# Performance work log

Measured on AMD Instinct MI355X. Metric: run time of the kernel, lower is better.

Reference implementation:

```python
import jax, jax.numpy as jnp
import numpy as np

H = W = 256
C = 128
SCALE = 512 ** (-0.5)  # literal from the source, not 1/sqrt(C)


def _pool_mat(size, out):
    # adaptive_avg_pool1d matrix: row i averages input[start_i:end_i]
    i = np.arange(out)
    s = (i * size) // out
    e = ((i + 1) * size + out - 1) // out  # ceil
    P = np.zeros((out, size), np.float32)
    for k in range(out):
        P[k, s[k]:e[k]] = 1.0 / (e[k] - s[k])
    return jnp.asarray(P)


def adaptive_avg_pool2d(x, out):
    # x: [B, C, H, W] -> [B, C, out, out] via separable pooling matrices
    Ph = _pool_mat(x.shape[2], out)
    Pw = _pool_mat(x.shape[3], out)
    y = jnp.einsum('oh,bchw->bcow', Ph, x)
    return jnp.einsum('pw,bcow->bcop', Pw, y)


def setup_inputs() -> dict:
    key = jax.random.key(0)
    k1, k2 = jax.random.split(key)
    x5 = jax.random.normal(k1, (4, C, H, W), dtype=jnp.float32)
    W_out = jax.random.normal(k2, (C, C), dtype=jnp.float32) * 0.02
    b_out = jnp.zeros((C,), dtype=jnp.float32)
    return {"x5": x5, "W_out": W_out, "b_out": b_out}


def reference(x5, W_out, b_out):
    B = x5.shape[0]
    # Query: [B, N, C], N = H*W
    Query = x5.reshape(B, C, H * W).transpose(0, 2, 1)
    # multi-scale pooled keys
    p16 = adaptive_avg_pool2d(x5, 16)
    p12 = adaptive_avg_pool2d(x5, 12)
    p9 = adaptive_avg_pool2d(x5, 9)
    p7 = adaptive_avg_pool2d(x5, 7)
    p6 = adaptive_avg_pool2d(x5, 6)
    p3 = adaptive_avg_pool2d(x5, 3)
    p1 = adaptive_avg_pool2d(x5, 1)
    # Key: concat flattened pools in source order [3, 1, 9, 7, 16] -> [B, C, 396]
    Key = jnp.concatenate(
        [p.reshape(B, C, -1) for p in (p3, p1, p9, p7, p16)], axis=-1)
    Value = Key.transpose(0, 2, 1)  # [B, 396, C]
    # attention: [B, N, 396]
    attn = jax.nn.softmax(SCALE * jnp.einsum('bnc,bck->bnk', Query, Key), axis=-1)
    agg = jnp.einsum('bnk,bkc->bnc', attn, Value)  # [B, N, C]
    agg = agg.transpose(0, 2, 1).reshape(B, C, H, W)
    # 1x1 conv
    out = jnp.einsum('oc,bchw->bohw', W_out, agg) + b_out[None, :, None, None]
    return (out + x5, p12, p6)
```

## Files before the change

### kernel.cpp

```cpp
#include <hip/hip_runtime.h>
#include <hip/hip_bf16.h>

typedef short bf16x8 __attribute__((ext_vector_type(8)));
typedef float f32x4  __attribute__((ext_vector_type(4)));
typedef unsigned short u16;

#define B_N 4
#define C_N 128
#define HW_ 256
#define NPIX 65536
#define NK 396
#define NKP 400
#define OUT_MAIN ((size_t)B_N * C_N * NPIX)
#define P12_OFF OUT_MAIN
#define P6_OFF  (P12_OFF + (size_t)B_N * C_N * 144)

#define BUFSZ  32768
#define VT_OFF 16384
#define LDS_BYTES 65536

static __device__ __forceinline__ u16 f2bf(float x) {
  __hip_bfloat16 h = __float2bfloat16(x);
  return *(u16*)&h;
}
static __device__ __forceinline__ unsigned pack2(float lo, float hi) {
  return ((unsigned)f2bf(hi) << 16) | f2bf(lo);
}
static __device__ __forceinline__ void gl_lds16(const void* g, void* l) {
  __builtin_amdgcn_global_load_lds(
      (const __attribute__((address_space(1))) unsigned*)g,
      (__attribute__((address_space(3))) unsigned*)l, 16, 0, 0);
}
#define MFMA32 __builtin_amdgcn_mfma_f32_16x16x32_bf16
#define BAR() do { __builtin_amdgcn_s_barrier(); \
                   __builtin_amdgcn_sched_barrier(0); } while (0)
#define VM8() do { asm volatile("s_waitcnt vmcnt(8)" ::: "memory"); \
                   __builtin_amdgcn_sched_barrier(0); } while (0)
#define VM4() do { asm volatile("s_waitcnt vmcnt(4)" ::: "memory"); \
                   __builtin_amdgcn_sched_barrier(0); } while (0)

template<int H0>
static __device__ __forceinline__ void pool_phaseA(
    const float2* __restrict__ plane2, float (*yh)[257], int w2)
{
  const int os_[7] = {16,12,9,7,6,3,1};
  const int ro_[7] = {0,16,28,37,44,50,53};
  float ax[7], ay[7], a2x[7], a2y[7], inv_[7];
  int r_[7], e_[7], s2_[7];
  #pragma unroll
  for (int s = 0; s < 7; ++s) {
    const int o = os_[s];
    const int r = (H0 * o) >> 8;
    const int sr = (r * 256) / o;
    r_[s]  = r;
    e_[s]  = ((r + 1) * 256 + o - 1) / o;
    s2_[s] = ((r + 1) * 256) / o;
    inv_[s] = 1.0f / (float)(e_[s] - sr);
    ax[s] = 0.f; ay[s] = 0.f; a2x[s] = 0.f; a2y[s] = 0.f;
  }
  #pragma unroll
  for (int g = 0; g < 4; ++g) {
    float2 vv[8];
    #pragma unroll
    for (int k = 0; k < 8; ++k) vv[k] = plane2[(H0 + g*8 + k) * 128 + w2];
    #pragma unroll
    for (int k = 0; k < 8; ++k) {
      const int h = H0 + g*8 + k;
      const float2 v = vv[k];
      #pragma unroll
      for (int s = 0; s < 7; ++s) {
        const int o = os_[s];
        ax[s] += v.x; ay[s] += v.y;
        if (h >= s2_[s]) { a2x[s] += v.x; a2y[s] += v.y; }
        if (h + 1 == e_[s]) {
          atomicAdd(&yh[ro_[s] + r_[s]][2*w2],     ax[s] * inv_[s]);
          atomicAdd(&yh[ro_[s] + r_[s]][2*w2 + 1], ay[s] * inv_[s]);
          r_[s]++;
          const int sr = s2_[s];
          e_[s]  = ((r_[s] + 1) * 256 + o - 1) / o;
          s2_[s] = ((r_[s] + 1) * 256) / o;
          inv_[s] = 1.0f / (float)(e_[s] - sr);
          ax[s] = a2x[s]; ay[s] = a2y[s];
          a2x[s] = 0.f; a2y[s] = 0.f;
        }
      }
    }
  }
  #pragma unroll
  for (int s = 0; s < 7; ++s) {
    const int o = os_[s];
    if (r_[s] < o) {
      atomicAdd(&yh[ro_[s] + r_[s]][2*w2],     ax[s] * inv_[s]);
      atomicAdd(&yh[ro_[s] + r_[s]][2*w2 + 1], ay[s] * inv_[s]);
      if (r_[s] + 1 < o && s2_[s] < H0 + 32) {
        const int sr2 = s2_[s];
        const int e2  = ((r_[s] + 2) * 256 + o - 1) / o;
        const float inv2 = 1.0f / (float)(e2 - sr2);
        atomicAdd(&yh[ro_[s] + r_[s] + 1][2*w2],     a2x[s] * inv2);
        atomicAdd(&yh[ro_[s] + r_[s] + 1][2*w2 + 1], a2y[s] * inv2);
      }
    }
  }
}

__global__ __launch_bounds__(1024) void pool_kernel(
    const float* __restrict__ x5, const float* __restrict__ W_out,
    u16* __restrict__ wsK, u16* __restrict__ wsKT, u16* __restrict__ wsW,
    float* __restrict__ out)
{
  __shared__ float yh[54][257];
  const int tid = threadIdx.x;
  const int bc = blockIdx.x;
  const int b  = bc >> 7;
  const int c  = bc & 127;
  const float2* plane2 = (const float2*)(x5 + (size_t)bc * NPIX);
  const int w2 = tid & 127;
  const int q  = tid >> 7;

  if (bc < 16) {
    const int idx = bc * 1024 + tid;
    const int o = idx >> 7, pp = idx & 127;
    const int q32 = pp >> 5, pos = pp & 31, g = pos >> 3, jj = pos & 7;
    const int csrc = q32 * 32 + ((jj < 4) ? (g * 4 + jj) : (16 + g * 4 + (jj - 4)));
    wsW[idx] = f2bf(W_out[o * 128 + csrc]);
  }

  for (int i = tid; i < 54 * 257; i += 1024) ((float*)yh)[i] = 0.f;
  __syncthreads();

  switch (q) {
    case 0: pool_phaseA<0>  (plane2, yh, w2); break;
    case 1: pool_phaseA<32> (plane2, yh, w2); break;
    case 2: pool_phaseA<64> (plane2, yh, w2); break;
    case 3: pool_phaseA<96> (plane2, yh, w2); break;
    case 4: pool_phaseA<128>(plane2, yh, w2); break;
    case 5: pool_phaseA<160>(plane2, yh, w2); break;
    case 6: pool_phaseA<192>(plane2, yh, w2); break;
    default: pool_phaseA<224>(plane2, yh, w2); break;
  }
  __syncthreads();

  if (tid < NKP - NK) {
    wsK [((size_t)b * NKP + NK + tid) * C_N + c] = 0;
    wsKT[(size_t)bc * NKP + NK + tid] = 0;
  }

  const int grp = tid >> 4;
  const int gl  = tid & 15;
  #pragma unroll
  for (int it = 0; it < 9; ++it) {
    const int r = grp + it * 64;
    int rr = r;
    int o, ro, kbase, dst;
    if      (rr < 256) { o = 16; ro = 0;  kbase = 140; dst = 0; }
    else if (rr < 400) { o = 12; ro = 16; kbase = 0;   dst = 1; rr -= 256; }
    else if (rr < 481) { o = 9;  ro = 28; kbase = 10;  dst = 0; rr -= 400; }
    else if (rr < 530) { o = 7;  ro = 37; kbase = 91;  dst = 0; rr -= 481; }
    else if (rr < 566) { o = 6;  ro = 44; kbase = 0;   dst = 2; rr -= 530; }
    else if (rr < 575) { o = 3;  ro = 50; kbase = 0;   dst = 0; rr -= 566; }
    else               { o = 1;  ro = 53; kbase = 9;   dst = 0; rr = 0;   }
    const int i = rr / o;
    const int j = rr - i * o;
    const int s = (j * HW_) / o;
    const int e = ((j + 1) * HW_ + o - 1) / o;
    float partial = 0.f;
    const float* row = yh[ro + i];
    for (int wq = s + gl; wq < e; wq += 16) partial += row[wq];
    partial += __shfl_xor(partial, 1);
    partial += __shfl_xor(partial, 2);
    partial += __shfl_xor(partial, 4);
    partial += __shfl_xor(partial, 8);
    if (gl == 0) {
      const float v = partial * (1.0f / (float)(e - s));
      if (dst == 1) {
        out[P12_OFF + (size_t)bc * 144 + rr] = v;
      } else if (dst == 2) {
        out[P6_OFF + (size_t)bc * 36 + rr] = v;
      } else {
        const int key = kbase + rr;
        const u16 bv = f2bf(v);
        wsK [((size_t)b * NKP + key) * C_N + c] = bv;
        wsKT[(size_t)bc * NKP + key]            = bv;
      }
    }
  }
}

template<int CB, int BUF>
static __device__ __forceinline__ void stage64(
    char* smem, const char* wsKb, const char* wsKTb, int wv, int lane)
{
  char* buf = smem + BUF * BUFSZ;
  const int lr = lane >> 4, lc = lane & 15;
  const int rit = wv * 4 + lr;
  #pragma unroll
  for (int j = 0; j < 4; ++j) {
    const int gk = CB + (j >> 1) * 32 + wv * 8 + ((j & 1) << 2) + lr;
    gl_lds16(wsKb + (size_t)gk * 256 + ((lc ^ rit) << 4),
             buf + j*4096 + wv*1024);
    const int vrow = j*32 + wv*8 + (lane >> 3);
    gl_lds16(wsKTb + (size_t)vrow * (NKP*2) + CB*2 + (((lane & 7) ^ (vrow & 7)) << 4),
             buf + VT_OFF + j*4096 + wv*1024);
  }
}

static __device__ __forceinline__ void stage_tail(
    char* buf, const char* wsKb, const char* wsKTb, int wv, int lane)
{
  const int lr = lane >> 4;
  const int rit = wv * 4 + lr;
  #pragma unroll
  for (int j = 0; j < 2; ++j) {
    const int gk = 384 + wv * 8 + (j << 2) + lr;
    gl_lds16(wsKb + (size_t)gk * 256 + (((lane & 15) ^ rit) << 4),
             buf + j*4096 + wv*1024);
  }
  #pragma unroll
  for (int j = 0; j < 2; ++j) {
    const int row = j*64 + wv*16 + (lane >> 2);
    gl_lds16(wsKTb + (size_t)row * (NKP*2) + 768 + ((lane & 3) << 4),
             buf + VT_OFF + j*4096 + wv*1024);
  }
}

static __device__ __forceinline__ void stage_W(
    char* smem, const u16* wsW, int wv, int lane)
{
  #pragma unroll
  for (int j = 0; j < 8; ++j) {
    const int row = j*16 + wv*4 + (lane >> 4);
    gl_lds16((const char*)wsW + (size_t)row * 256 + (((lane & 15) ^ (row & 15)) << 4),
             smem + BUFSZ + j*4096 + wv*1024);
  }
}

template<int BUF, int TAIL>
static __device__ __forceinline__ void compute64(
    char* smem, const bf16x8 (&qf)[2][4],
    f32x4 (&agg)[8][2], float (&d)[2], int l15, int l4)
{
  const char* buf = smem + BUF * BUFSZ;
  constexpr int NT   = TAIL ? 2 : 4;
  constexpr int SUBS = TAIL ? 1 : 2;

  f32x4 sA[NT][2];
  #pragma unroll
  for (int nt = 0; nt < NT; ++nt) {
    sA[nt][0] = (f32x4){0.f,0.f,0.f,0.f};
    sA[nt][1] = (f32x4){0.f,0.f,0.f,0.f};
  }
  #pragma unroll
  for (int nt = 0; nt < NT; ++nt) {
    bf16x8 kf[4];
    #pragma unroll
    for (int kc = 0; kc < 4; ++kc)
      kf[kc] = *(const bf16x8*)(buf + (nt*16 + l15) * 256 +
                                ((kc*64 + l4*16) ^ (l15 << 4)));
    #pragma unroll
    for (int kc = 0; kc < 4; ++kc) {
      sA[nt][0] = MFMA32(kf[kc], qf[0][kc], sA[nt][0], 0, 0, 0);
      sA[nt][1] = MFMA32(kf[kc], qf[1][kc], sA[nt][1], 0, 0, 0);
    }
  }

  #pragma unroll
  for (int sub = 0; sub < SUBS; ++sub) {
    bf16x8 pf[2];
    #pragma unroll
    for (int pt = 0; pt < 2; ++pt) {
      float e[8];
      #pragma unroll
      for (int qi = 0; qi < 4; ++qi) e[qi]     = exp2f(sA[2*sub][pt][qi]);
      #pragma unroll
      for (int qi = 0; qi < 4; ++qi) e[4 + qi] = exp2f(sA[2*sub + 1][pt][qi]);
      if (TAIL) {
        #pragma unroll
        for (int j = 0; j < 8; ++j) if (l4*8 + j >= 12) e[j] = 0.f;
      }
      d[pt] += ((e[0]+e[1]) + (e[2]+e[3])) + ((e[4]+e[5]) + (e[6]+e[7]));
      bf16x8 t;
      #pragma unroll
      for (int j = 0; j < 8; ++j) t[j] = (short)f2bf(e[j]);
      pf[pt] = t;
    }
    #pragma unroll
    for (int ct = 0; ct < 8; ++ct) {
      const int vrow = ct*16 + l15;
      bf16x8 vf;
      if (TAIL)
        vf = *(const bf16x8*)(buf + VT_OFF + vrow*64 + l4*16);
      else
        vf = *(const bf16x8*)(buf + VT_OFF + vrow*128 +
                              ((sub*64 + l4*16) ^ ((vrow & 7) << 4)));
      agg[ct][0] = MFMA32(vf, pf[0], agg[ct][0], 0, 0, 0);
      agg[ct][1] = MFMA32(vf, pf[1], agg[ct][1], 0, 0, 0);
    }
  }
}

__global__ __launch_bounds__(256, 2) void attn_kernel(
    const float* __restrict__ x5, const u16* __restrict__ wsK,
    const u16* __restrict__ wsKT, const u16* __restrict__ wsW,
    const float* __restrict__ b_out, float* __restrict__ out)
{
  extern __shared__ char smem[];
  const int tid  = threadIdx.x;
  const int wgid = (blockIdx.x & 7) * 256 + (blockIdx.x >> 3);
  const int b    = wgid >> 9;
  const int pix0 = (wgid & 511) << 7;
  const int lane = tid & 63, wv = tid >> 6;
  const int l15  = lane & 15, l4 = lane >> 4;
  const float SCL2 = 0.044194173824159216f * 1.4426950408889634f;

  const char* wsKb  = (const char*)wsK  + (size_t)b * NKP * C_N * 2;
  const char* wsKTb = (const char*)wsKT + (size_t)b * C_N * NKP * 2;

  {
    const float* r0p = x5 + (((size_t)(b * C_N + 2*lane)) << 16) + pix0 + wv * 32;
    const float* r1p = r0p + NPIX;
    float4 v0[8], v1[8];
    #pragma unroll
    for (int j = 0; j < 8; ++j) {
      v0[j] = *(const float4*)(r0p + j*4);
      v1[j] = *(const float4*)(r1p + j*4);
    }
    #pragma unroll
    for (int i = 0; i < 32; ++i) {
      const int pix = wv * 32 + i;
      const unsigned pk = pack2(((const float*)&v0[i>>2])[i&3] * SCL2,
                                ((const float*)&v1[i>>2])[i&3] * SCL2);
      *(unsigned*)(smem + pix * 256 + ((lane*4) ^ ((pix & 15) << 4))) = pk;
    }
  }
  __syncthreads();

  bf16x8 qf[2][4];
  #pragma unroll
  for (int pt = 0; pt < 2; ++pt)
    #pragma unroll
    for (int kc = 0; kc < 4; ++kc)
      qf[pt][kc] = *(const bf16x8*)(smem + (wv*32 + pt*16 + l15) * 256 +
                                    ((kc*64 + l4*16) ^ (l15 << 4)));
  __syncthreads();

  f32x4 agg[8][2];
  #pragma unroll
  for (int ct = 0; ct < 8; ++ct) {
    agg[ct][0] = (f32x4){0.f,0.f,0.f,0.f};
    agg[ct][1] = (f32x4){0.f,0.f,0.f,0.f};
  }
  float d[2] = {0.f, 0.f};

  stage64<0, 0>(smem, wsKb, wsKTb, wv, lane);
  stage64<64, 1>(smem, wsKb, wsKTb, wv, lane);
  VM8(); BAR();
  compute64<0, 0>(smem, qf, agg, d, l15, l4);
  BAR();

  stage64<128, 0>(smem, wsKb, wsKTb, wv, lane);
  VM8(); BAR();
  compute64<1, 0>(smem, qf, agg, d, l15, l4);
  BAR();

  stage64<192, 1>(smem, wsKb, wsKTb, wv, lane);
  VM8(); BAR();
  compute64<0, 0>(smem, qf, agg, d, l15, l4);
  BAR();

  stage64<256, 0>(smem, wsKb, wsKTb, wv, lane);
  VM8(); BAR();
  compute64<1, 0>(smem, qf, agg, d, l15, l4);
  BAR();

  stage64<320, 1>(smem, wsKb, wsKTb, wv, lane);
  VM8(); BAR();
  compute64<0, 0>(smem, qf, agg, d, l15, l4);
  BAR();

  stage_tail(smem, wsKb, wsKTb, wv, lane);
  VM4(); BAR();
  compute64<1, 0>(smem, qf, agg, d, l15, l4);
  BAR();

  stage_W(smem, wsW, wv, lane);
  asm volatile("s_waitcnt vmcnt(0)" ::: "memory");
  __syncthreads();

  compute64<0, 1>(smem, qf, agg, d, l15, l4);

  float inv[2];
  #pragma unroll
  for (int pt = 0; pt < 2; ++pt) {
    float s = d[pt];
    s += __shfl_xor(s, 16);
    s += __shfl_xor(s, 32);
    inv[pt] = 1.0f / s;
  }

  f32x4 cacc[8][2];
  #pragma unroll
  for (int ot = 0; ot < 8; ++ot) {
    cacc[ot][0] = (f32x4){0.f,0.f,0.f,0.f};
    cacc[ot][1] = (f32x4){0.f,0.f,0.f,0.f};
  }
  #pragma unroll
  for (int qh = 0; qh < 4; ++qh) {
    bf16x8 agf[2];
    #pragma unroll
    for (int pt = 0; pt < 2; ++pt) {
      bf16x8 t;
      #pragma unroll
      for (int j = 0; j < 8; ++j)
        t[j] = (short)f2bf(agg[2*qh + (j >> 2)][pt][j & 3] * inv[pt]);
      agf[pt] = t;
    }
    #pragma unroll
    for (int ot = 0; ot < 8; ++ot) {
      const bf16x8 wa = *(const bf16x8*)(smem + BUFSZ + (ot*16 + l15) * 256 +
                                         ((qh*64 + l4*16) ^ (l15 << 4)));
      cacc[ot][0] = MFMA32(wa, agf[0], cacc[ot][0], 0, 0, 0);
      cacc[ot][1] = MFMA32(wa, agf[1], cacc[ot][1], 0, 0, 0);
    }
  }

  #pragma unroll
  for (int ot = 0; ot < 8; ++ot) {
    const float4 bq = *(const float4*)(b_out + ot*16 + l4*4);
    #pragma unroll
    for (int pt = 0; pt < 2; ++pt) {
      #pragma unroll
      for (int qi = 0; qi < 4; ++qi) {
        const int o = ot*16 + l4*4 + qi;
        const size_t idx = (((size_t)(b * C_N + o)) << 16) + pix0 + wv*32 + pt*16 + l15;
        out[idx] = cacc[ot][pt][qi] + ((const float*)&bq)[qi] + x5[idx];
      }
    }
  }
}

extern "C" void kernel_launch(void* const* d_in, const int* in_sizes, int n_in,
                              void* d_out, int out_size, void* d_ws, size_t ws_size,
                              hipStream_t stream) {
  const float* x5    = (const float*)d_in[0];
  const float* W_out = (const float*)d_in[1];
  const float* b_out = (const float*)d_in[2];
  float* out = (float*)d_out;
  u16* wsKT = (u16*)d_ws;
  u16* wsK  = (u16*)((char*)d_ws + (size_t)B_N * C_N * NKP * 2);
  u16* wsW  = (u16*)((char*)d_ws + (size_t)2 * B_N * C_N * NKP * 2);

  pool_kernel<<<512, 1024, 0, stream>>>(x5, W_out, wsK, wsKT, wsW, out);

  hipFuncSetAttribute((const void*)attn_kernel,
                      hipFuncAttributeMaxDynamicSharedMemorySize, LDS_BYTES);
  attn_kernel<<<B_N * 512, 256, LDS_BYTES, stream>>>(x5, wsK, wsKT, wsW, b_out, out);
}
```

Before: 182.2 us.

## Double attention workgroup to 8 waves sharing each staged K/V tile

Each attention workgroup grows from 4 to 8 waves and from 128 to 256 pixels, and the grid is halved. Each K/V chunk staged into LDS is now reused by twice as many waves, so every wave issues half as many global-to-LDS loads. The staging loops and vmcnt waits are redistributed to match. The launch bound becomes (512, 4), which asks for more waves per SIMD and so caps registers per thread harder; that risks spills of the large accumulator and Q fragment arrays, and LDS may still limit how many workgroups fit on a CU.

```diff
diff --git a/kernel.cpp b/kernel.cpp
--- a/kernel.cpp
+++ b/kernel.cpp
@@ -34,9 +34,9 @@
 #define MFMA32 __builtin_amdgcn_mfma_f32_16x16x32_bf16
 #define BAR() do { __builtin_amdgcn_s_barrier(); \
                    __builtin_amdgcn_sched_barrier(0); } while (0)
-#define VM8() do { asm volatile("s_waitcnt vmcnt(8)" ::: "memory"); \
+#define VM4() do { asm volatile("s_waitcnt vmcnt(4)" ::: "memory"); \
                    __builtin_amdgcn_sched_barrier(0); } while (0)
-#define VM4() do { asm volatile("s_waitcnt vmcnt(4)" ::: "memory"); \
+#define VM2() do { asm volatile("s_waitcnt vmcnt(2)" ::: "memory"); \
                    __builtin_amdgcn_sched_barrier(0); } while (0)
 
 template<int H0>
@@ -192,45 +192,53 @@
 {
   char* buf = smem + BUF * BUFSZ;
   const int lr = lane >> 4, lc = lane & 15;
-  const int rit = wv * 4 + lr;
-  #pragma unroll
-  for (int j = 0; j < 4; ++j) {
-    const int gk = CB + (j >> 1) * 32 + wv * 8 + ((j & 1) << 2) + lr;
+  #pragma unroll
+  for (int t = 0; t < 2; ++t) {
+    const int op  = wv * 2 + t;
+    const int j   = op >> 2;
+    const int rb  = (op & 3) * 4;
+    const int rit = rb + lr;
+    const int gk  = CB + (j >> 1) * 32 + 8 * (rb >> 2) + ((j & 1) << 2) + lr;
     gl_lds16(wsKb + (size_t)gk * 256 + ((lc ^ rit) << 4),
-             buf + j*4096 + wv*1024);
-    const int vrow = j*32 + wv*8 + (lane >> 3);
+             buf + j * 4096 + rb * 256);
+    const int vrow = op * 8 + (lane >> 3);
     gl_lds16(wsKTb + (size_t)vrow * (NKP*2) + CB*2 + (((lane & 7) ^ (vrow & 7)) << 4),
-             buf + VT_OFF + j*4096 + wv*1024);
+             buf + VT_OFF + op * 1024);
   }
 }
 
 static __device__ __forceinline__ void stage_tail(
     char* buf, const char* wsKb, const char* wsKTb, int wv, int lane)
 {
-  const int lr = lane >> 4;
-  const int rit = wv * 4 + lr;
-  #pragma unroll
-  for (int j = 0; j < 2; ++j) {
-    const int gk = 384 + wv * 8 + (j << 2) + lr;
-    gl_lds16(wsKb + (size_t)gk * 256 + (((lane & 15) ^ rit) << 4),
-             buf + j*4096 + wv*1024);
-  }
-  #pragma unroll
-  for (int j = 0; j < 2; ++j) {
-    const int row = j*64 + wv*16 + (lane >> 2);
-    gl_lds16(wsKTb + (size_t)row * (NKP*2) + 768 + ((lane & 3) << 4),
-             buf + VT_OFF + j*4096 + wv*1024);
+  const int lr = lane >> 4, lc = lane & 15;
+  #pragma unroll
+  for (int t = 0; t < 2; ++t) {
+    const int op = wv * 2 + t;
+    if (op < 8) {
+      const int j = op >> 2, rb = (op & 3) * 4;
+      const int rit = rb + lr;
+      const int gk = 384 + 8 * (rb >> 2) + ((j & 1) << 2) + lr;
+      gl_lds16(wsKb + (size_t)gk * 256 + ((lc ^ rit) << 4),
+               buf + j * 4096 + rb * 256);
+    } else {
+      const int v = op - 8;
+      const int row = v * 16 + (lane >> 2);
+      gl_lds16(wsKTb + (size_t)row * (NKP*2) + 768 + ((lane & 3) << 4),
+               buf + VT_OFF + v * 1024);
+    }
   }
 }
 
 static __device__ __forceinline__ void stage_W(
     char* smem, const u16* wsW, int wv, int lane)
 {
-  #pragma unroll
-  for (int j = 0; j < 8; ++j) {
-    const int row = j*16 + wv*4 + (lane >> 4);
-    gl_lds16((const char*)wsW + (size_t)row * 256 + (((lane & 15) ^ (row & 15)) << 4),
-             smem + BUFSZ + j*4096 + wv*1024);
+  const int lr = lane >> 4, lc = lane & 15;
+  #pragma unroll
+  for (int t = 0; t < 4; ++t) {
+    const int op = wv * 4 + t;
+    const int row = op * 4 + lr;
+    gl_lds16((const char*)wsW + (size_t)row * 256 + ((lc ^ (row & 15)) << 4),
+             smem + BUFSZ + op * 1024);
   }
 }
 
@@ -298,16 +306,16 @@
   }
 }
 
-__global__ __launch_bounds__(256, 2) void attn_kernel(
+__global__ __launch_bounds__(512, 4) void attn_kernel(
     const float* __restrict__ x5, const u16* __restrict__ wsK,
     const u16* __restrict__ wsKT, const u16* __restrict__ wsW,
     const float* __restrict__ b_out, float* __restrict__ out)
 {
   extern __shared__ char smem[];
   const int tid  = threadIdx.x;
-  const int wgid = (blockIdx.x & 7) * 256 + (blockIdx.x >> 3);
-  const int b    = wgid >> 9;
-  const int pix0 = (wgid & 511) << 7;
+  const int wgid = (blockIdx.x & 7) * 128 + (blockIdx.x >> 3);
+  const int b    = wgid >> 8;
+  const int pix0 = (wgid & 255) << 8;
   const int lane = tid & 63, wv = tid >> 6;
   const int l15  = lane & 15, l4 = lane >> 4;
   const float SCL2 = 0.044194173824159216f * 1.4426950408889634f;
@@ -353,32 +361,32 @@
 
   stage64<0, 0>(smem, wsKb, wsKTb, wv, lane);
   stage64<64, 1>(smem, wsKb, wsKTb, wv, lane);
-  VM8(); BAR();
+  VM4(); BAR();
   compute64<0, 0>(smem, qf, agg, d, l15, l4);
   BAR();
 
   stage64<128, 0>(smem, wsKb, wsKTb, wv, lane);
-  VM8(); BAR();
+  VM4(); BAR();
   compute64<1, 0>(smem, qf, agg, d, l15, l4);
   BAR();
 
   stage64<192, 1>(smem, wsKb, wsKTb, wv, lane);
-  VM8(); BAR();
+  VM4(); BAR();
   compute64<0, 0>(smem, qf, agg, d, l15, l4);
   BAR();
 
   stage64<256, 0>(smem, wsKb, wsKTb, wv, lane);
-  VM8(); BAR();
+  VM4(); BAR();
   compute64<1, 0>(smem, qf, agg, d, l15, l4);
   BAR();
 
   stage64<320, 1>(smem, wsKb, wsKTb, wv, lane);
-  VM8(); BAR();
+  VM4(); BAR();
   compute64<0, 0>(smem, qf, agg, d, l15, l4);
   BAR();
 
   stage_tail(smem, wsKb, wsKTb, wv, lane);
-  VM4(); BAR();
+  VM2(); BAR();
   compute64<1, 0>(smem, qf, agg, d, l15, l4);
   BAR();
 
@@ -453,5 +461,5 @@
 
   hipFuncSetAttribute((const void*)attn_kernel,
                       hipFuncAttributeMaxDynamicSharedMemorySize, LDS_BYTES);
-  attn_kernel<<<B_N * 512, 256, LDS_BYTES, stream>>>(x5, wsK, wsKT, wsW, b_out, out);
-}
+  attn_kernel<<<B_N * 256, 512, LDS_BYTES, stream>>>(x5, wsK, wsKT, wsW, b_out, out);
+}
```

Result: slower. 585.2 us (+221.2%).

## Process two 128-pixel query tiles per workgroup to reuse staged keys

Applied to the files above, without the earlier changes.

Each workgroup now handles 256 pixels as two query tiles, so every staged K/V chunk and the output weight matrix loaded into LDS serves twice as many queries. The grid is halved to 1024 workgroups. This cuts global and LDS staging traffic per pixel. In exchange each thread holds two sets of accumulators and query fragments, which roughly doubles register use and may force spills or lower occupancy under the 2-wave launch bound.

```diff
diff --git a/kernel.cpp b/kernel.cpp
--- a/kernel.cpp
+++ b/kernel.cpp
@@ -305,9 +305,9 @@
 {
   extern __shared__ char smem[];
   const int tid  = threadIdx.x;
-  const int wgid = (blockIdx.x & 7) * 256 + (blockIdx.x >> 3);
-  const int b    = wgid >> 9;
-  const int pix0 = (wgid & 511) << 7;
+  const int wgid = (blockIdx.x & 7) * 128 + (blockIdx.x >> 3);
+  const int b    = wgid >> 8;
+  const int pix0 = (wgid & 255) << 8;
   const int lane = tid & 63, wv = tid >> 6;
   const int l15  = lane & 15, l4 = lane >> 4;
   const float SCL2 = 0.044194173824159216f * 1.4426950408889634f;
@@ -315,8 +315,11 @@
   const char* wsKb  = (const char*)wsK  + (size_t)b * NKP * C_N * 2;
   const char* wsKTb = (const char*)wsKT + (size_t)b * C_N * NKP * 2;
 
-  {
-    const float* r0p = x5 + (((size_t)(b * C_N + 2*lane)) << 16) + pix0 + wv * 32;
+  bf16x8 qfA[2][4], qfB[2][4];
+  #pragma unroll
+  for (int tile = 0; tile < 2; ++tile) {
+    const float* r0p = x5 + (((size_t)(b * C_N + 2*lane)) << 16) + pix0 +
+                       tile * 128 + wv * 32;
     const float* r1p = r0p + NPIX;
     float4 v0[8], v1[8];
     #pragma unroll
@@ -331,108 +334,127 @@
                                 ((const float*)&v1[i>>2])[i&3] * SCL2);
       *(unsigned*)(smem + pix * 256 + ((lane*4) ^ ((pix & 15) << 4))) = pk;
     }
-  }
-  __syncthreads();
-
-  bf16x8 qf[2][4];
-  #pragma unroll
-  for (int pt = 0; pt < 2; ++pt)
-    #pragma unroll
-    for (int kc = 0; kc < 4; ++kc)
-      qf[pt][kc] = *(const bf16x8*)(smem + (wv*32 + pt*16 + l15) * 256 +
-                                    ((kc*64 + l4*16) ^ (l15 << 4)));
-  __syncthreads();
-
-  f32x4 agg[8][2];
+    __syncthreads();
+    #pragma unroll
+    for (int pt = 0; pt < 2; ++pt)
+      #pragma unroll
+      for (int kc = 0; kc < 4; ++kc) {
+        const bf16x8 v = *(const bf16x8*)(smem + (wv*32 + pt*16 + l15) * 256 +
+                                          ((kc*64 + l4*16) ^ (l15 << 4)));
+        if (tile == 0) qfA[pt][kc] = v; else qfB[pt][kc] = v;
+      }
+    __syncthreads();
+  }
+
+  f32x4 aggA[8][2], aggB[8][2];
   #pragma unroll
   for (int ct = 0; ct < 8; ++ct) {
-    agg[ct][0] = (f32x4){0.f,0.f,0.f,0.f};
-    agg[ct][1] = (f32x4){0.f,0.f,0.f,0.f};
-  }
-  float d[2] = {0.f, 0.f};
+    aggA[ct][0] = (f32x4){0.f,0.f,0.f,0.f};
+    aggA[ct][1] = (f32x4){0.f,0.f,0.f,0.f};
+    aggB[ct][0] = (f32x4){0.f,0.f,0.f,0.f};
+    aggB[ct][1] = (f32x4){0.f,0.f,0.f,0.f};
+  }
+  float dA[2] = {0.f, 0.f}, dB[2] = {0.f, 0.f};
 
   stage64<0, 0>(smem, wsKb, wsKTb, wv, lane);
   stage64<64, 1>(smem, wsKb, wsKTb, wv, lane);
   VM8(); BAR();
-  compute64<0, 0>(smem, qf, agg, d, l15, l4);
+  compute64<0, 0>(smem, qfA, aggA, dA, l15, l4);
+  compute64<0, 0>(smem, qfB, aggB, dB, l15, l4);
   BAR();
 
   stage64<128, 0>(smem, wsKb, wsKTb, wv, lane);
   VM8(); BAR();
-  compute64<1, 0>(smem, qf, agg, d, l15, l4);
+  compute64<1, 0>(smem, qfA, aggA, dA, l15, l4);
+  compute64<1, 0>(smem, qfB, aggB, dB, l15, l4);
   BAR();
 
   stage64<192, 1>(smem, wsKb, wsKTb, wv, lane);
   VM8(); BAR();
-  compute64<0, 0>(smem, qf, agg, d, l15, l4);
+  compute64<0, 0>(smem, qfA, aggA, dA, l15, l4);
+  compute64<0, 0>(smem, qfB, aggB, dB, l15, l4);
   BAR();
 
   stage64<256, 0>(smem, wsKb, wsKTb, wv, lane);
   VM8(); BAR();
-  compute64<1, 0>(smem, qf, agg, d, l15, l4);
+  compute64<1, 0>(smem, qfA, aggA, dA, l15, l4);
+  compute64<1, 0>(smem, qfB, aggB, dB, l15, l4);
   BAR();
 
   stage64<320, 1>(smem, wsKb, wsKTb, wv, lane);
   VM8(); BAR();
-  compute64<0, 0>(smem, qf, agg, d, l15, l4);
+  compute64<0, 0>(smem, qfA, aggA, dA, l15, l4);
+  compute64<0, 0>(smem, qfB, aggB, dB, l15, l4);
   BAR();
 
   stage_tail(smem, wsKb, wsKTb, wv, lane);
   VM4(); BAR();
-  compute64<1, 0>(smem, qf, agg, d, l15, l4);
+  compute64<1, 0>(smem, qfA, aggA, dA, l15, l4);
+  compute64<1, 0>(smem, qfB, aggB, dB, l15, l4);
   BAR();
 
   stage_W(smem, wsW, wv, lane);
   asm volatile("s_waitcnt vmcnt(0)" ::: "memory");
   __syncthreads();
 
-  compute64<0, 1>(smem, qf, agg, d, l15, l4);
-
-  float inv[2];
+  compute64<0, 1>(smem, qfA, aggA, dA, l15, l4);
+  compute64<0, 1>(smem, qfB, aggB, dB, l15, l4);
+
+  float invA[2], invB[2];
   #pragma unroll
   for (int pt = 0; pt < 2; ++pt) {
-    float s = d[pt];
+    float s = dA[pt];
     s += __shfl_xor(s, 16);
     s += __shfl_xor(s, 32);
-    inv[pt] = 1.0f / s;
-  }
-
-  f32x4 cacc[8][2];
-  #pragma unroll
-  for (int ot = 0; ot < 8; ++ot) {
-    cacc[ot][0] = (f32x4){0.f,0.f,0.f,0.f};
-    cacc[ot][1] = (f32x4){0.f,0.f,0.f,0.f};
-  }
-  #pragma unroll
-  for (int qh = 0; qh < 4; ++qh) {
-    bf16x8 agf[2];
-    #pragma unroll
-    for (int pt = 0; pt < 2; ++pt) {
-      bf16x8 t;
-      #pragma unroll
-      for (int j = 0; j < 8; ++j)
-        t[j] = (short)f2bf(agg[2*qh + (j >> 2)][pt][j & 3] * inv[pt]);
-      agf[pt] = t;
-    }
+    invA[pt] = 1.0f / s;
+    float s2 = dB[pt];
+    s2 += __shfl_xor(s2, 16);
+    s2 += __shfl_xor(s2, 32);
+    invB[pt] = 1.0f / s2;
+  }
+
+  #pragma unroll
+  for (int tile = 0; tile < 2; ++tile) {
+    f32x4 cacc[8][2];
     #pragma unroll
     for (int ot = 0; ot < 8; ++ot) {
-      const bf16x8 wa = *(const bf16x8*)(smem + BUFSZ + (ot*16 + l15) * 256 +
-                                         ((qh*64 + l4*16) ^ (l15 << 4)));
-      cacc[ot][0] = MFMA32(wa, agf[0], cacc[ot][0], 0, 0, 0);
-      cacc[ot][1] = MFMA32(wa, agf[1], cacc[ot][1], 0, 0, 0);
-    }
-  }
-
-  #pragma unroll
-  for (int ot = 0; ot < 8; ++ot) {
-    const float4 bq = *(const float4*)(b_out + ot*16 + l4*4);
-    #pragma unroll
-    for (int pt = 0; pt < 2; ++pt) {
-      #pragma unroll
-      for (int qi = 0; qi < 4; ++qi) {
-        const int o = ot*16 + l4*4 + qi;
-        const size_t idx = (((size_t)(b * C_N + o)) << 16) + pix0 + wv*32 + pt*16 + l15;
-        out[idx] = cacc[ot][pt][qi] + ((const float*)&bq)[qi] + x5[idx];
+      cacc[ot][0] = (f32x4){0.f,0.f,0.f,0.f};
+      cacc[ot][1] = (f32x4){0.f,0.f,0.f,0.f};
+    }
+    #pragma unroll
+    for (int qh = 0; qh < 4; ++qh) {
+      bf16x8 agf[2];
+      #pragma unroll
+      for (int pt = 0; pt < 2; ++pt) {
+        bf16x8 t;
+        #pragma unroll
+        for (int j = 0; j < 8; ++j) {
+          const float a = tile ? aggB[2*qh + (j >> 2)][pt][j & 3] * invB[pt]
+                               : aggA[2*qh + (j >> 2)][pt][j & 3] * invA[pt];
+          t[j] = (short)f2bf(a);
+        }
+        agf[pt] = t;
+      }
+      #pragma unroll
+      for (int ot = 0; ot < 8; ++ot) {
+        const bf16x8 wa = *(const bf16x8*)(smem + BUFSZ + (ot*16 + l15) * 256 +
+                                           ((qh*64 + l4*16) ^ (l15 << 4)));
+        cacc[ot][0] = MFMA32(wa, agf[0], cacc[ot][0], 0, 0, 0);
+        cacc[ot][1] = MFMA32(wa, agf[1], cacc[ot][1], 0, 0, 0);
+      }
+    }
+    #pragma unroll
+    for (int ot = 0; ot < 8; ++ot) {
+      const float4 bq = *(const float4*)(b_out + ot*16 + l4*4);
+      #pragma unroll
+      for (int pt = 0; pt < 2; ++pt) {
+        #pragma unroll
+        for (int qi = 0; qi < 4; ++qi) {
+          const int o = ot*16 + l4*4 + qi;
+          const size_t idx = (((size_t)(b * C_N + o)) << 16) + pix0 +
+                             tile * 128 + wv*32 + pt*16 + l15;
+          out[idx] = cacc[ot][pt][qi] + ((const float*)&bq)[qi] + x5[idx];
+        }
       }
     }
   }
@@ -453,5 +475,5 @@
 
   hipFuncSetAttribute((const void*)attn_kernel,
                       hipFuncAttributeMaxDynamicSharedMemorySize, LDS_BYTES);
-  attn_kernel<<<B_N * 512, 256, LDS_BYTES, stream>>>(x5, wsK, wsKT, wsW, b_out, out);
-}
+  attn_kernel<<<B_N * 256, 256, LDS_BYTES, stream>>>(x5, wsK, wsKT, wsW, b_out, out);
+}
```

New measurement: 516.0 us. 2.83x slower.
